# Kernel optimization log

Measured on AMD Instinct MI355X. Metric: run time of the kernel, lower is better.

The kernel has to match this reference:

```python
import jax, jax.numpy as jnp
import numpy as np

ROPE_BASE = 10000.0
NEG_INF = jnp.finfo(jnp.float32).min


def _rope_tables(T, head_dim):
    inv_freq = 1.0 / (ROPE_BASE ** (jnp.arange(0, head_dim, 2, dtype=jnp.float32) / head_dim))
    t = jnp.arange(T, dtype=jnp.float32)
    freqs = jnp.einsum('i,j->ij', t, inv_freq)          # [T, head_dim/2]
    emb = jnp.concatenate([freqs, freqs], axis=-1)      # [T, head_dim]
    return jnp.cos(emb), jnp.sin(emb)


def _rotate_half(x):
    d = x.shape[-1] // 2
    return jnp.concatenate([-x[..., d:], x[..., :d]], axis=-1)


def setup_inputs() -> dict:
    key = jax.random.key(0)
    ks = jax.random.split(key, 6)
    B, T, C = 2, 2048, 1024
    s = 0.02
    return {
        'x': jax.random.normal(ks[0], (B, T, C), jnp.float32),
        'attn_mask': jnp.ones((B, T), jnp.int32),
        'wq': jax.random.normal(ks[1], (C, C), jnp.float32) * s,
        'wk': jax.random.normal(ks[2], (C, C), jnp.float32) * s,
        'wv': jax.random.normal(ks[3], (C, C), jnp.float32) * s,
        'wo': jax.random.normal(ks[4], (C, C), jnp.float32) * s,
        'bo': jnp.zeros((C,), jnp.float32),
        'is_causal': 1,
    }


def reference(x, attn_mask, wq, wk, wv, wo, bo, is_causal):
    B, T, C = x.shape
    H = 16
    D = C // H

    q = (x @ wq).reshape(B, T, H, D).transpose(0, 2, 1, 3)  # [B,H,T,D]
    k = (x @ wk).reshape(B, T, H, D).transpose(0, 2, 1, 3)
    v = (x @ wv).reshape(B, T, H, D).transpose(0, 2, 1, 3)

    # inline RoPE (self-attention path); note scaling_factor = 1.0 in this branch,
    # faithful to the original module.
    cos, sin = _rope_tables(T, D)            # [T, D]
    cos = cos[None, None]                    # [1,1,T,D]
    sin = sin[None, None]
    q = q * cos + _rotate_half(q) * sin
    k = k * cos + _rotate_half(k) * sin

    scores = jnp.einsum('bhqd,bhkd->bhqk', q, k)  # [B,H,T,T], scale 1.0 w/ RoPE

    # mask union: padding mask (2D attn_mask) OR causal mask
    pad_mask = ~(attn_mask.astype(bool))[:, None, None, :]            # [B,1,1,T]
    causal = jnp.triu(jnp.ones((T, T), bool), k=1)[None, None]        # [1,1,T,T]
    if is_causal:
        final_mask = pad_mask | causal
    else:
        final_mask = pad_mask
    scores = jnp.where(final_mask, NEG_INF, scores)

    attn = jax.nn.softmax(scores, axis=-1)   # dropout omitted (eval mode)
    out = jnp.einsum('bhqk,bhkd->bhqd', attn, v)
    out = out.transpose(0, 2, 1, 3).reshape(B, T, C)
    return out @ wo + bo
```

## Files before the change

kernel.cpp:

```cpp
#include <hip/hip_runtime.h>
#include <hip/hip_bf16.h>
#include <stdint.h>

#define B_ 2
#define T_ 2048
#define C_ 1024
#define H_ 16
#define D_ 64
#define NEG_INF_F (-3.4028234663852886e38f)

typedef __bf16 bf16;
typedef __bf16 bf16x4 __attribute__((ext_vector_type(4)));
typedef __bf16 bf16x8 __attribute__((ext_vector_type(8)));
typedef float  f32x4  __attribute__((ext_vector_type(4)));

__device__ __forceinline__ void gload16(const bf16* g, bf16* l) {
  __builtin_amdgcn_global_load_lds(
      (const __attribute__((address_space(1))) void*)(g),
      (__attribute__((address_space(3))) void*)(l), 16, 0, 0);
}

__device__ __forceinline__ f32x4 mfma16(bf16x8 a, bf16x8 b, f32x4 c) {
  return __builtin_amdgcn_mfma_f32_16x16x32_bf16(a, b, c, 0, 0, 0);
}


__global__ void k_prep_x(const float* __restrict__ x, bf16* __restrict__ xb) {
  int i = (blockIdx.x * 256 + threadIdx.x) * 4;
  float4 v = *(const float4*)(x + i);
  bf16x4 o;
  o[0] = (bf16)v.x; o[1] = (bf16)v.y; o[2] = (bf16)v.z; o[3] = (bf16)v.w;
  *(bf16x4*)(xb + i) = o;
}

__global__ void k_prep_wrm(const float* __restrict__ wq, const float* __restrict__ wk,
                           const float* __restrict__ wv, const float* __restrict__ wo,
                           bf16* __restrict__ wqkvT, bf16* __restrict__ woT,
                           float* __restrict__ rc, float* __restrict__ rs,
                           const int* __restrict__ amask, float* __restrict__ negm,
                           unsigned char* __restrict__ tileclean) {
  __shared__ float tile[32][33];
  const int mat = blockIdx.z;
  const int tid = threadIdx.x;
  if (mat < 4) {
    const float* src = (mat == 0) ? wq : (mat == 1) ? wk : (mat == 2) ? wv : wo;
    bf16* dst = (mat < 3) ? (wqkvT + (size_t)mat * C_ * C_) : woT;
    int k0 = blockIdx.y * 32, n0 = blockIdx.x * 32;
    int tx = tid & 31, ty = tid >> 5;
    #pragma unroll
    for (int r = 0; r < 32; r += 8)
      tile[ty + r][tx] = src[(size_t)(k0 + ty + r) * C_ + n0 + tx];
    __syncthreads();
    #pragma unroll
    for (int r = 0; r < 32; r += 8)
      dst[(size_t)(n0 + ty + r) * C_ + k0 + tx] = (bf16)tile[tx][ty + r];
    return;
  }
  const int flat = blockIdx.y * 32 + blockIdx.x;
  if (flat < 256) {
    int i = flat * 256 + tid;
    int t = i >> 5, d = i & 31;
    float inv = expf(-(float)(2 * d) * (9.210340371976184f / 64.0f));
    float fr = (float)t * inv;
    rc[i] = cosf(fr);
    rs[i] = sinf(fr);
  } else if (flat < 256 + B_) {
    int b = flat - 256;
    int base = b * T_ + tid * 8;
    int4 a0 = *(const int4*)(amask + base);
    int4 a1 = *(const int4*)(amask + base + 4);
    bool ok = a0.x && a0.y && a0.z && a0.w && a1.x && a1.y && a1.z && a1.w;
    float4 f0, f1;
    f0.x = a0.x ? 0.f : NEG_INF_F; f0.y = a0.y ? 0.f : NEG_INF_F;
    f0.z = a0.z ? 0.f : NEG_INF_F; f0.w = a0.w ? 0.f : NEG_INF_F;
    f1.x = a1.x ? 0.f : NEG_INF_F; f1.y = a1.y ? 0.f : NEG_INF_F;
    f1.z = a1.z ? 0.f : NEG_INF_F; f1.w = a1.w ? 0.f : NEG_INF_F;
    *(float4*)(negm + base) = f0;
    *(float4*)(negm + base + 4) = f1;
    unsigned long long m = __ballot(ok);
    int w = tid >> 6, lane = tid & 63;
    if (lane < 8) {
      tileclean[b * 32 + w * 8 + lane] =
          (unsigned char)(((m >> (lane * 8)) & 0xFFull) == 0xFFull);
    }
  }
}

template <int MODE, int BM>
__global__ __launch_bounds__(256, 2)
void k_gemm(const bf16* __restrict__ A, const bf16* __restrict__ BT,
            const float* __restrict__ rc, const float* __restrict__ rs,
            bf16* __restrict__ qb, bf16* __restrict__ kbuf, bf16* __restrict__ vtb,
            const float* __restrict__ bo, float* __restrict__ outp) {
  constexpr int K = C_;
  constexpr int MI = BM / 32;
  constexpr int NT = (MODE == 0) ? 24 : 8;
  constexpr int MCH = (MODE == 0) ? 4 : 8;
  __shared__ __align__(16) bf16 lA[BM * 64];
  __shared__ __align__(16) bf16 lB[128 * 64];
  const int tid = threadIdx.x;
  const int bid = blockIdx.x;
  const int xcd = bid & 7, idx = bid >> 3;
  const int mt = xcd * MCH + idx / NT;
  const int nt = idx % NT;
  const int m0 = mt * BM, n0 = nt * 128;
  const int lane = tid & 63, w = tid >> 6;
  const int l15 = lane & 15, g = lane >> 4;
  const int wm = (w >> 1) * (BM / 2), wn = (w & 1) * 64;

  f32x4 acc[MI][4] = {};

  const int srow = tid >> 3;
  const int scb = (tid & 7) ^ (srow & 7);
  const bf16* gA = A + (size_t)(m0 + srow) * K + scb * 8;
  const bf16* gB = BT + (size_t)(n0 + srow) * K + scb * 8;
  bf16* sA = lA + tid * 8;
  bf16* sB = lB + tid * 8;
  const int swl = l15 & 7;

  for (int k0 = 0; k0 < K; k0 += 64) {
    #pragma unroll
    for (int i = 0; i < BM / 32; i++)
      gload16(gA + (size_t)(i * 32) * K + k0, sA + i * 2048);
    #pragma unroll
    for (int i = 0; i < 4; i++)
      gload16(gB + (size_t)(i * 32) * K + k0, sB + i * 2048);
    __syncthreads();

    #pragma unroll
    for (int kk = 0; kk < 2; kk++) {
      bf16x8 af[MI], bfr[4];
      const int pcb = ((kk * 4 + g) ^ swl) << 3;
      #pragma unroll
      for (int i = 0; i < MI; i++)
        af[i] = *(const bf16x8*)(lA + (wm + i * 16 + l15) * 64 + pcb);
      #pragma unroll
      for (int j = 0; j < 4; j++)
        bfr[j] = *(const bf16x8*)(lB + (wn + j * 16 + l15) * 64 + pcb);
      #pragma unroll
      for (int i = 0; i < MI; i++)
        #pragma unroll
        for (int j = 0; j < 4; j++)
          acc[i][j] = mfma16(af[i], bfr[j], acc[i][j]);
    }
    __syncthreads();
  }

  if constexpr (MODE == 0) {
    const int region = n0 >> 10;
    const int nr = (n0 & 1023) + wn;
    const int h = nr >> 6;
    if (region < 2) {
      bf16* dst = (region == 0) ? qb : kbuf;
      #pragma unroll
      for (int i = 0; i < MI; i++) {
        #pragma unroll
        for (int r = 0; r < 4; r++) {
          int m = m0 + wm + i * 16 + g * 4 + r;
          int b = m >> 11, t = m & 2047;
          size_t base = ((size_t)(b * H_ + h) * T_ + t) * 64;
          #pragma unroll
          for (int j = 0; j < 2; j++) {
            int dl = j * 16 + l15;
            float c = rc[t * 32 + dl], s = rs[t * 32 + dl];
            float lo = acc[i][j][r], hi = acc[i][j + 2][r];
            dst[base + dl]      = (bf16)(lo * c - hi * s);
            dst[base + dl + 32] = (bf16)(hi * c + lo * s);
          }
        }
      }
    } else {
      #pragma unroll
      for (int i = 0; i < MI; i++)
        #pragma unroll
        for (int j = 0; j < 4; j++) {
          int d = j * 16 + l15;
          #pragma unroll
          for (int r = 0; r < 4; r++) {
            int m = m0 + wm + i * 16 + g * 4 + r;
            int b = m >> 11, t = m & 2047;
            vtb[((size_t)(b * H_ + h) * 64 + d) * T_ + t] = (bf16)acc[i][j][r];
          }
        }
    }
  } else {
    #pragma unroll
    for (int i = 0; i < MI; i++)
      #pragma unroll
      for (int j = 0; j < 4; j++) {
        int n = n0 + wn + j * 16 + l15;
        float bias = bo[n];
        #pragma unroll
        for (int r = 0; r < 4; r++) {
          int m = m0 + wm + i * 16 + g * 4 + r;
          outp[(size_t)m * C_ + n] = acc[i][j][r] + bias;
        }
      }
  }
}

__global__ __launch_bounds__(256, 4)
void k_attn(const bf16* __restrict__ qb, const bf16* __restrict__ kbuf,
            const bf16* __restrict__ vtb, const float* __restrict__ negm,
            const unsigned char* __restrict__ tileclean,
            const int* __restrict__ pcausal, bf16* __restrict__ ob) {
  __shared__ __align__(16) bf16 lK[2][64 * 64];
  __shared__ __align__(16) bf16 lV[2][64 * 64];
  __shared__ __align__(16) bf16 lP[4][16 * 64];
  const int bx = blockIdx.x;
  const int qi = 31 - (bx >> 5);
  const int bh = bx & 31;
  const int b = bh >> 4, h = bh & 15;
  const int causal = pcausal[0];
  const int tid = threadIdx.x, lane = tid & 63, w = tid >> 6;
  const int l15 = lane & 15, g = lane >> 4;
  const int sw7 = l15 & 7;
  const int q0 = qi * 64;
  const int wq0 = q0 + w * 16;
  const size_t plane = (size_t)(b * H_ + h) * T_ * 64;

  const int nkt = causal ? (qi + 1) : (T_ / 64);

  unsigned int bits = 0;
  {
    const unsigned char* tcb = tileclean + b * 32;
    #pragma unroll
    for (int i2 = 0; i2 < 32; i2++) bits |= ((unsigned int)tcb[i2]) << i2;
  }

  bf16x8 qf[2];
  #pragma unroll
  for (int kf = 0; kf < 2; kf++)
    qf[kf] = *(const bf16x8*)(qb + plane + (size_t)(wq0 + l15) * 64 + kf * 32 + g * 8);

  f32x4 o[4] = {};
  float psum[4] = {0.f, 0.f, 0.f, 0.f};

  const int srow = tid >> 3;
  const int skb = tid & 7;
  const int scol = ((skb ^ (srow & 7)) << 3);
  const bf16* gK = kbuf + plane + (size_t)srow * 64 + scol;
  const bf16* gV = vtb + plane + (size_t)srow * T_ + scol;
  bf16* myP = lP[w];

  {
    bf16* sKd = lK[0] + tid * 8;
    bf16* sVd = lV[0] + tid * 8;
    gload16(gK, sKd);
    gload16(gK + (size_t)32 * 64, sKd + 2048);
    gload16(gV, sVd);
    gload16(gV + (size_t)32 * T_, sVd + 2048);
  }
  __syncthreads();

  int cur = 0;
  for (int kt = 0; kt < nkt; kt++) {
    if (kt + 1 < nkt) {
      const size_t nk0 = (size_t)(kt + 1) * 64;
      bf16* sKd = lK[cur ^ 1] + tid * 8;
      bf16* sVd = lV[cur ^ 1] + tid * 8;
      gload16(gK + nk0 * 64, sKd);
      gload16(gK + (nk0 + 32) * 64, sKd + 2048);
      gload16(gV + nk0, sVd);
      gload16(gV + (size_t)32 * T_ + nk0, sVd + 2048);
    }
    __builtin_amdgcn_sched_barrier(0);

    const bf16* cK = lK[cur];
    const bf16* cV = lV[cur];
    const size_t k0 = (size_t)kt * 64;

    f32x4 s[4] = {};
    #pragma unroll
    for (int j = 0; j < 4; j++) {
      const int kr = j * 16 + l15;
      bf16x8 k0f = *(const bf16x8*)(cK + kr * 64 + (((0 + g) ^ sw7) << 3));
      bf16x8 k1f = *(const bf16x8*)(cK + kr * 64 + (((4 + g) ^ sw7) << 3));
      s[j] = mfma16(qf[0], k0f, s[j]);
      s[j] = mfma16(qf[1], k1f, s[j]);
    }

    if (!((bits >> kt) & 1)) {
      #pragma unroll
      for (int j = 0; j < 4; j++) {
        float nm = negm[b * T_ + (int)k0 + j * 16 + l15];
        #pragma unroll
        for (int r = 0; r < 4; r++) s[j][r] += nm;
      }
    }
    if (causal && (kt == nkt - 1)) {
      #pragma unroll
      for (int j = 0; j < 4; j++) {
        const int kkg = (int)k0 + j * 16 + l15;
        #pragma unroll
        for (int r = 0; r < 4; r++) {
          const int qg = wq0 + g * 4 + r;
          if (kkg > qg) s[j][r] = NEG_INF_F;
        }
      }
    }

    #pragma unroll
    for (int r = 0; r < 4; r++) {
      float p0 = __expf(s[0][r]), p1 = __expf(s[1][r]);
      float p2 = __expf(s[2][r]), p3 = __expf(s[3][r]);
      s[0][r] = p0; s[1][r] = p1; s[2][r] = p2; s[3][r] = p3;
      psum[r] += (p0 + p1) + (p2 + p3);
    }

    #pragma unroll
    for (int j = 0; j < 4; j++) {
      const int col = j * 16 + l15;
      const int kb2 = col >> 3, c7 = col & 7;
      #pragma unroll
      for (int r = 0; r < 4; r++) {
        const int rw = g * 4 + r;
        myP[rw * 64 + ((kb2 ^ (rw & 7)) << 3) + c7] = (bf16)s[j][r];
      }
    }

    #pragma unroll
    for (int kt2 = 0; kt2 < 2; kt2++) {
      bf16x8 pa = *(const bf16x8*)(myP + l15 * 64 + (((kt2 * 4 + g) ^ sw7) << 3));
      #pragma unroll
      for (int df = 0; df < 4; df++) {
        bf16x8 bv = *(const bf16x8*)(cV + (df * 16 + l15) * 64 + (((kt2 * 4 + g) ^ sw7) << 3));
        o[df] = mfma16(pa, bv, o[df]);
      }
    }

    __syncthreads();
    cur ^= 1;
  }

  float inv[4];
  #pragma unroll
  for (int r = 0; r < 4; r++) {
    float t = psum[r];
    t += __shfl_xor(t, 1);
    t += __shfl_xor(t, 2);
    t += __shfl_xor(t, 4);
    t += __shfl_xor(t, 8);
    inv[r] = 1.0f / t;
  }
  #pragma unroll
  for (int df = 0; df < 4; df++) {
    const int d = df * 16 + l15;
    #pragma unroll
    for (int r = 0; r < 4; r++) {
      const int t = wq0 + g * 4 + r;
      ob[((size_t)(b * T_ + t)) * C_ + h * 64 + d] = (bf16)(o[df][r] * inv[r]);
    }
  }
}

extern "C" void kernel_launch(void* const* d_in, const int* in_sizes, int n_in,
                              void* d_out, int out_size, void* d_ws, size_t ws_size,
                              hipStream_t stream) {
  const float* x  = (const float*)d_in[0];
  const int* amask = (const int*)d_in[1];
  const float* wq = (const float*)d_in[2];
  const float* wk = (const float*)d_in[3];
  const float* wv = (const float*)d_in[4];
  const float* wo = (const float*)d_in[5];
  const float* bo = (const float*)d_in[6];
  const int* isc  = (const int*)d_in[7];
  float* outp = (float*)d_out;

  char* ws = (char*)d_ws;
  bf16* xb    = (bf16*)(ws);
  bf16* wqkvT = (bf16*)(ws + ((size_t)8 << 20));
  bf16* woT   = (bf16*)(ws + ((size_t)14 << 20));
  float* rc   = (float*)(ws + ((size_t)16 << 20));
  float* rs   = (float*)(ws + ((size_t)16 << 20) + (256 << 10));
  float* negm = (float*)(ws + ((size_t)16 << 20) + (512 << 10));
  unsigned char* tileclean = (unsigned char*)(ws + ((size_t)16 << 20) + (528 << 10));
  bf16* qbuf  = (bf16*)(ws + ((size_t)17 << 20));
  bf16* kbuf  = (bf16*)(ws + ((size_t)25 << 20));
  bf16* vtbuf = (bf16*)(ws + ((size_t)33 << 20));
  bf16* obuf  = (bf16*)(ws + ((size_t)41 << 20));

  hipLaunchKernelGGL(k_prep_x, dim3(4096), dim3(256), 0, stream, x, xb);
  hipLaunchKernelGGL(k_prep_wrm, dim3(32, 32, 5), dim3(256), 0, stream,
                     wq, wk, wv, wo, wqkvT, woT, rc, rs, amask, negm, tileclean);
  hipLaunchKernelGGL((k_gemm<0, 128>), dim3(768), dim3(256), 0, stream,
                     xb, wqkvT, rc, rs, qbuf, kbuf, vtbuf, nullptr, nullptr);
  hipLaunchKernelGGL(k_attn, dim3(1024), dim3(256), 0, stream,
                     qbuf, kbuf, vtbuf, negm, tileclean, isc, obuf);
  hipLaunchKernelGGL((k_gemm<1, 64>), dim3(512), dim3(256), 0, stream,
                     obuf, woT, nullptr, nullptr, nullptr, nullptr, nullptr, bo, outp);
}
```

Measured before the change: 178.4 us.

## Rewrite attention with 32x32 MFMA, register-resident P and exp2 softmax

The attention kernel moves to 128-thread blocks of two waves. Each wave handles 32 query rows with 32x32x16 MFMAs and computes S transposed, so the probabilities can be packed to bf16 and rearranged with permlane32 swaps. This removes the LDS round-trip for P. The log2(e) factor is folded into the Q RoPE epilogue so exp2f replaces __expf, and the output GEMM switches to BM=32 with twice as many blocks. The cost is fewer waves per block for latency hiding, more registers per thread, and a smaller-tile output GEMM.

```diff
diff --git a/kernel.cpp b/kernel.cpp
--- a/kernel.cpp
+++ b/kernel.cpp
@@ -8,11 +8,14 @@
 #define H_ 16
 #define D_ 64
 #define NEG_INF_F (-3.4028234663852886e38f)
+#define LOG2E_F 1.44269504088896340736f
 
 typedef __bf16 bf16;
 typedef __bf16 bf16x4 __attribute__((ext_vector_type(4)));
 typedef __bf16 bf16x8 __attribute__((ext_vector_type(8)));
 typedef float  f32x4  __attribute__((ext_vector_type(4)));
+typedef float  f32x16 __attribute__((ext_vector_type(16)));
+typedef uint32_t u32x4 __attribute__((ext_vector_type(4)));
 
 __device__ __forceinline__ void gload16(const bf16* g, bf16* l) {
   __builtin_amdgcn_global_load_lds(
@@ -22,6 +25,9 @@
 
 __device__ __forceinline__ f32x4 mfma16(bf16x8 a, bf16x8 b, f32x4 c) {
   return __builtin_amdgcn_mfma_f32_16x16x32_bf16(a, b, c, 0, 0, 0);
+}
+__device__ __forceinline__ f32x16 mfma32(bf16x8 a, bf16x8 b, f32x16 c) {
+  return __builtin_amdgcn_mfma_f32_32x32x16_bf16(a, b, c, 0, 0, 0);
 }
 
 
@@ -95,7 +101,7 @@
   constexpr int K = C_;
   constexpr int MI = BM / 32;
   constexpr int NT = (MODE == 0) ? 24 : 8;
-  constexpr int MCH = (MODE == 0) ? 4 : 8;
+  constexpr int MCH = (MODE == 0) ? 4 : 16;
   __shared__ __align__(16) bf16 lA[BM * 64];
   __shared__ __align__(16) bf16 lB[128 * 64];
   const int tid = threadIdx.x;
@@ -152,6 +158,7 @@
     const int h = nr >> 6;
     if (region < 2) {
       bf16* dst = (region == 0) ? qb : kbuf;
+      const float sc = (region == 0) ? LOG2E_F : 1.0f;
       #pragma unroll
       for (int i = 0; i < MI; i++) {
         #pragma unroll
@@ -162,7 +169,7 @@
           #pragma unroll
           for (int j = 0; j < 2; j++) {
             int dl = j * 16 + l15;
-            float c = rc[t * 32 + dl], s = rs[t * 32 + dl];
+            float c = rc[t * 32 + dl] * sc, s = rs[t * 32 + dl] * sc;
             float lo = acc[i][j][r], hi = acc[i][j + 2][r];
             dst[base + dl]      = (bf16)(lo * c - hi * s);
             dst[base + dl + 32] = (bf16)(hi * c + lo * s);
@@ -199,26 +206,23 @@
   }
 }
 
-__global__ __launch_bounds__(256, 4)
+__global__ __launch_bounds__(128, 2)
 void k_attn(const bf16* __restrict__ qb, const bf16* __restrict__ kbuf,
             const bf16* __restrict__ vtb, const float* __restrict__ negm,
             const unsigned char* __restrict__ tileclean,
             const int* __restrict__ pcausal, bf16* __restrict__ ob) {
   __shared__ __align__(16) bf16 lK[2][64 * 64];
   __shared__ __align__(16) bf16 lV[2][64 * 64];
-  __shared__ __align__(16) bf16 lP[4][16 * 64];
   const int bx = blockIdx.x;
   const int qi = 31 - (bx >> 5);
   const int bh = bx & 31;
   const int b = bh >> 4, h = bh & 15;
   const int causal = pcausal[0];
-  const int tid = threadIdx.x, lane = tid & 63, w = tid >> 6;
-  const int l15 = lane & 15, g = lane >> 4;
-  const int sw7 = l15 & 7;
-  const int q0 = qi * 64;
-  const int wq0 = q0 + w * 16;
+  const int tid = threadIdx.x, lane = tid & 63, wid = tid >> 6;
+  const int l31 = lane & 31, hi = lane >> 5;
+  const int sw7 = l31 & 7;
+  const int wq0 = qi * 64 + wid * 32;
   const size_t plane = (size_t)(b * H_ + h) * T_ * 64;
-
   const int nkt = causal ? (qi + 1) : (T_ / 64);
 
   unsigned int bits = 0;
@@ -228,28 +232,27 @@
     for (int i2 = 0; i2 < 32; i2++) bits |= ((unsigned int)tcb[i2]) << i2;
   }
 
-  bf16x8 qf[2];
+  bf16x8 qf[4];
   #pragma unroll
-  for (int kf = 0; kf < 2; kf++)
-    qf[kf] = *(const bf16x8*)(qb + plane + (size_t)(wq0 + l15) * 64 + kf * 32 + g * 8);
-
-  f32x4 o[4] = {};
-  float psum[4] = {0.f, 0.f, 0.f, 0.f};
+  for (int ds = 0; ds < 4; ds++)
+    qf[ds] = *(const bf16x8*)(qb + plane + (size_t)(wq0 + l31) * 64 + ds * 16 + hi * 8);
+
+  f32x16 o0 = {}, o1 = {};
+  float psum = 0.f;
 
   const int srow = tid >> 3;
-  const int skb = tid & 7;
-  const int scol = ((skb ^ (srow & 7)) << 3);
+  const int scol = (((tid & 7) ^ (srow & 7)) << 3);
   const bf16* gK = kbuf + plane + (size_t)srow * 64 + scol;
   const bf16* gV = vtb + plane + (size_t)srow * T_ + scol;
-  bf16* myP = lP[w];
 
   {
     bf16* sKd = lK[0] + tid * 8;
     bf16* sVd = lV[0] + tid * 8;
-    gload16(gK, sKd);
-    gload16(gK + (size_t)32 * 64, sKd + 2048);
-    gload16(gV, sVd);
-    gload16(gV + (size_t)32 * T_, sVd + 2048);
+    #pragma unroll
+    for (int i = 0; i < 4; i++) {
+      gload16(gK + (size_t)(i * 16) * 64, sKd + i * 1024);
+      gload16(gV + (size_t)(i * 16) * T_, sVd + i * 1024);
+    }
   }
   __syncthreads();
 
@@ -259,73 +262,79 @@
       const size_t nk0 = (size_t)(kt + 1) * 64;
       bf16* sKd = lK[cur ^ 1] + tid * 8;
       bf16* sVd = lV[cur ^ 1] + tid * 8;
-      gload16(gK + nk0 * 64, sKd);
-      gload16(gK + (nk0 + 32) * 64, sKd + 2048);
-      gload16(gV + nk0, sVd);
-      gload16(gV + (size_t)32 * T_ + nk0, sVd + 2048);
+      #pragma unroll
+      for (int i = 0; i < 4; i++) {
+        gload16(gK + (nk0 + i * 16) * 64, sKd + i * 1024);
+        gload16(gV + (size_t)(i * 16) * T_ + nk0, sVd + i * 1024);
+      }
     }
     __builtin_amdgcn_sched_barrier(0);
 
     const bf16* cK = lK[cur];
     const bf16* cV = lV[cur];
-    const size_t k0 = (size_t)kt * 64;
-
-    f32x4 s[4] = {};
-    #pragma unroll
-    for (int j = 0; j < 4; j++) {
-      const int kr = j * 16 + l15;
-      bf16x8 k0f = *(const bf16x8*)(cK + kr * 64 + (((0 + g) ^ sw7) << 3));
-      bf16x8 k1f = *(const bf16x8*)(cK + kr * 64 + (((4 + g) ^ sw7) << 3));
-      s[j] = mfma16(qf[0], k0f, s[j]);
-      s[j] = mfma16(qf[1], k1f, s[j]);
+    const int k0 = kt * 64;
+
+    f32x16 st0 = {}, st1 = {};
+    #pragma unroll
+    for (int ds = 0; ds < 4; ds++) {
+      const int slot = ((ds * 2 + hi) ^ sw7) << 3;
+      bf16x8 a0 = *(const bf16x8*)(cK + (0 + l31) * 64 + slot);
+      bf16x8 a1 = *(const bf16x8*)(cK + (32 + l31) * 64 + slot);
+      st0 = mfma32(a0, qf[ds], st0);
+      st1 = mfma32(a1, qf[ds], st1);
     }
 
     if (!((bits >> kt) & 1)) {
       #pragma unroll
-      for (int j = 0; j < 4; j++) {
-        float nm = negm[b * T_ + (int)k0 + j * 16 + l15];
-        #pragma unroll
-        for (int r = 0; r < 4; r++) s[j][r] += nm;
+      for (int r = 0; r < 16; r++) {
+        const int cr = (r & 3) + 8 * (r >> 2) + 4 * hi;
+        st0[r] += negm[b * T_ + k0 + cr] * LOG2E_F;
+        st1[r] += negm[b * T_ + k0 + 32 + cr] * LOG2E_F;
       }
     }
     if (causal && (kt == nkt - 1)) {
       #pragma unroll
-      for (int j = 0; j < 4; j++) {
-        const int kkg = (int)k0 + j * 16 + l15;
-        #pragma unroll
-        for (int r = 0; r < 4; r++) {
-          const int qg = wq0 + g * 4 + r;
-          if (kkg > qg) s[j][r] = NEG_INF_F;
+      for (int r = 0; r < 16; r++) {
+        const int cr = (r & 3) + 8 * (r >> 2) + 4 * hi;
+        const int qg = wq0 + l31;
+        if (k0 + cr > qg)      st0[r] = NEG_INF_F;
+        if (k0 + 32 + cr > qg) st1[r] = NEG_INF_F;
+      }
+    }
+
+    #pragma unroll
+    for (int r = 0; r < 16; r++) {
+      float p0 = exp2f(st0[r]), p1 = exp2f(st1[r]);
+      st0[r] = p0; st1[r] = p1;
+      psum += p0 + p1;
+    }
+
+    #pragma unroll
+    for (int t = 0; t < 2; t++) {
+      #pragma unroll
+      for (int s = 0; s < 2; s++) {
+        uint32_t wA, wB, wC, wD;
+        if (t == 0) {
+          asm("v_cvt_pk_bf16_f32 %0, %1, %2" : "=v"(wA) : "v"(st0[8*s+0]), "v"(st0[8*s+1]));
+          asm("v_cvt_pk_bf16_f32 %0, %1, %2" : "=v"(wB) : "v"(st0[8*s+4]), "v"(st0[8*s+5]));
+          asm("v_cvt_pk_bf16_f32 %0, %1, %2" : "=v"(wC) : "v"(st0[8*s+2]), "v"(st0[8*s+3]));
+          asm("v_cvt_pk_bf16_f32 %0, %1, %2" : "=v"(wD) : "v"(st0[8*s+6]), "v"(st0[8*s+7]));
+        } else {
+          asm("v_cvt_pk_bf16_f32 %0, %1, %2" : "=v"(wA) : "v"(st1[8*s+0]), "v"(st1[8*s+1]));
+          asm("v_cvt_pk_bf16_f32 %0, %1, %2" : "=v"(wB) : "v"(st1[8*s+4]), "v"(st1[8*s+5]));
+          asm("v_cvt_pk_bf16_f32 %0, %1, %2" : "=v"(wC) : "v"(st1[8*s+2]), "v"(st1[8*s+3]));
+          asm("v_cvt_pk_bf16_f32 %0, %1, %2" : "=v"(wD) : "v"(st1[8*s+6]), "v"(st1[8*s+7]));
         }
-      }
-    }
-
-    #pragma unroll
-    for (int r = 0; r < 4; r++) {
-      float p0 = __expf(s[0][r]), p1 = __expf(s[1][r]);
-      float p2 = __expf(s[2][r]), p3 = __expf(s[3][r]);
-      s[0][r] = p0; s[1][r] = p1; s[2][r] = p2; s[3][r] = p3;
-      psum[r] += (p0 + p1) + (p2 + p3);
-    }
-
-    #pragma unroll
-    for (int j = 0; j < 4; j++) {
-      const int col = j * 16 + l15;
-      const int kb2 = col >> 3, c7 = col & 7;
-      #pragma unroll
-      for (int r = 0; r < 4; r++) {
-        const int rw = g * 4 + r;
-        myP[rw * 64 + ((kb2 ^ (rw & 7)) << 3) + c7] = (bf16)s[j][r];
-      }
-    }
-
-    #pragma unroll
-    for (int kt2 = 0; kt2 < 2; kt2++) {
-      bf16x8 pa = *(const bf16x8*)(myP + l15 * 64 + (((kt2 * 4 + g) ^ sw7) << 3));
-      #pragma unroll
-      for (int df = 0; df < 4; df++) {
-        bf16x8 bv = *(const bf16x8*)(cV + (df * 16 + l15) * 64 + (((kt2 * 4 + g) ^ sw7) << 3));
-        o[df] = mfma16(pa, bv, o[df]);
+        asm("v_permlane32_swap_b32 %0, %1" : "+v"(wA), "+v"(wB));
+        asm("v_permlane32_swap_b32 %0, %1" : "+v"(wC), "+v"(wD));
+        u32x4 pw = {wA, wC, wB, wD};
+        bf16x8 pa = __builtin_bit_cast(bf16x8, pw);
+        const int ks = t * 2 + s;
+        const int slot = ((ks * 2 + hi) ^ sw7) << 3;
+        bf16x8 bv0 = *(const bf16x8*)(cV + (0 + l31) * 64 + slot);
+        bf16x8 bv1 = *(const bf16x8*)(cV + (32 + l31) * 64 + slot);
+        o0 = mfma32(pa, bv0, o0);
+        o1 = mfma32(pa, bv1, o1);
       }
     }
 
@@ -333,24 +342,18 @@
     cur ^= 1;
   }
 
-  float inv[4];
+  float tot = psum + __shfl_xor(psum, 32);
+  float inv = 1.0f / tot;
+  float* lInv = (float*)lK + wid * 32;
+  if (hi == 0) lInv[l31] = inv;
+  __builtin_amdgcn_wave_barrier();
   #pragma unroll
-  for (int r = 0; r < 4; r++) {
-    float t = psum[r];
-    t += __shfl_xor(t, 1);
-    t += __shfl_xor(t, 2);
-    t += __shfl_xor(t, 4);
-    t += __shfl_xor(t, 8);
-    inv[r] = 1.0f / t;
-  }
-  #pragma unroll
-  for (int df = 0; df < 4; df++) {
-    const int d = df * 16 + l15;
-    #pragma unroll
-    for (int r = 0; r < 4; r++) {
-      const int t = wq0 + g * 4 + r;
-      ob[((size_t)(b * T_ + t)) * C_ + h * 64 + d] = (bf16)(o[df][r] * inv[r]);
-    }
+  for (int r = 0; r < 16; r++) {
+    const int cr = (r & 3) + 8 * (r >> 2) + 4 * hi;
+    const float ir = lInv[cr];
+    const size_t row = (size_t)(b * T_ + wq0 + cr) * C_ + h * 64;
+    ob[row + l31]      = (bf16)(o0[r] * ir);
+    ob[row + 32 + l31] = (bf16)(o1[r] * ir);
   }
 }
 
@@ -385,8 +388,8 @@
                      wq, wk, wv, wo, wqkvT, woT, rc, rs, amask, negm, tileclean);
   hipLaunchKernelGGL((k_gemm<0, 128>), dim3(768), dim3(256), 0, stream,
                      xb, wqkvT, rc, rs, qbuf, kbuf, vtbuf, nullptr, nullptr);
-  hipLaunchKernelGGL(k_attn, dim3(1024), dim3(256), 0, stream,
+  hipLaunchKernelGGL(k_attn, dim3(1024), dim3(128), 0, stream,
                      qbuf, kbuf, vtbuf, negm, tileclean, isc, obuf);
-  hipLaunchKernelGGL((k_gemm<1, 64>), dim3(512), dim3(256), 0, stream,
+  hipLaunchKernelGGL((k_gemm<1, 32>), dim3(1024), dim3(256), 0, stream,
                      obuf, woT, nullptr, nullptr, nullptr, nullptr, nullptr, bo, outp);
 }
```

Measured after the change: 187.9 us. +5.3%, slower.
